# Optimization experiments

Hardware: AMD Instinct MI355X
Metric: run time of the kernel (lower is better)

## Reference

```python
import jax, jax.numpy as jnp
import numpy as np

HEADS = 12
HEAD_DIM = 64
WINDOW = 65  # must be odd
EMBED = 768
B, L = 1, 2048


def setup_inputs() -> dict:
    key = jax.random.key(0)
    k1, k2, k3 = jax.random.split(key, 3)
    x = jax.random.normal(k1, (B, L, EMBED), dtype=jnp.float32)
    w_qkv = jax.random.normal(k2, (EMBED, 3 * HEADS * HEAD_DIM), dtype=jnp.float32) * 0.02
    w_out = jax.random.normal(k3, (HEADS * HEAD_DIM, EMBED), dtype=jnp.float32) * 0.02
    b_out = jnp.zeros((EMBED,), dtype=jnp.float32)
    return {"x": x, "w_qkv": w_qkv, "w_out": w_out, "b_out": b_out}


def reference(x, w_qkv, w_out, b_out):
    b, l, _ = x.shape
    pad = WINDOW // 2
    # qkv projection (no bias), reshape to [B, L, H, 3*Dh], split as in TF code
    qkv = jnp.einsum('ble,ef->blf', x, w_qkv).reshape(b, l, HEADS, 3 * HEAD_DIM)
    q = qkv[..., :HEAD_DIM]                      # [B, L, H, Dh]
    k = qkv[..., HEAD_DIM:2 * HEAD_DIM]
    v = qkv[..., 2 * HEAD_DIM:]
    # zero-pad along sequence (matches tf.pad; padded positions participate in softmax)
    k_pad = jnp.pad(k, ((0, 0), (pad, pad), (0, 0), (0, 0)))  # [B, L+2p, H, Dh]
    v_pad = jnp.pad(v, ((0, 0), (pad, pad), (0, 0), (0, 0)))
    # sliding windows via a single gather: [B, L, W, H, Dh]
    idx = jnp.arange(l)[:, None] + jnp.arange(WINDOW)[None, :]
    k_win = k_pad[:, idx]
    v_win = v_pad[:, idx]
    score = jnp.einsum('blhd,blwhd->blhw', q, k_win) / jnp.sqrt(
        jnp.asarray(HEAD_DIM, dtype=x.dtype))
    weights = jax.nn.softmax(score, axis=-1)      # [B, L, H, W]
    out = jnp.einsum('blhw,blwhd->blhd', weights, v_win)
    out = out.reshape(b, l, HEADS * HEAD_DIM)
    return jnp.einsum('blf,fe->ble', out, w_out) + b_out
```

## Files before the change

### kernel.cpp

```cpp
#include <hip/hip_runtime.h>
#include <hip/hip_bf16.h>

#define HEADS 12
#define HD 64
#define PADW 32
#define EMBED 768
#define LSEQ 2048
#define QKV_N (3 * HEADS * HD)
#define LPAD (LSEQ + 64)

typedef short short8 __attribute__((ext_vector_type(8)));
typedef short short4v __attribute__((ext_vector_type(4)));
typedef float f32x4 __attribute__((ext_vector_type(4)));

__device__ short g_xb[LSEQ * EMBED];
__device__ short g_wqkvT[QKV_N * EMBED];
__device__ short g_woutT[EMBED * EMBED];
__device__ short g_qkvb[LSEQ * QKV_N];
__device__ short g_vT[HEADS * HD * LPAD];
__device__ short g_attnb[LSEQ * EMBED];

__device__ __forceinline__ short f2bf(float f) {
  unsigned x = __builtin_bit_cast(unsigned, f);
  x += 0x7fffu + ((x >> 16) & 1u);
  return (short)(x >> 16);
}

#define GLB(p) ((const __attribute__((address_space(1))) void*)(p))
#define LDS(p) ((__attribute__((address_space(3))) void*)(p))

#define PREP_A 1536
#define PREP_B 1728
#define PREP_C 576
#define PREP_D 24
#define PREP_TOT (PREP_A + PREP_B + PREP_C + PREP_D)

__global__ __launch_bounds__(256) void prep(
    const float* __restrict__ x, const float* __restrict__ w_qkv,
    const float* __restrict__ w_out, short* __restrict__ xb,
    short* __restrict__ wqkvT, short* __restrict__ woutT,
    short* __restrict__ vT) {
  __shared__ float T[32][33];
  const int b = blockIdx.x, tid = threadIdx.x;
  if (b < PREP_A) {
    int i = b * 256 + tid;
    float4 v = ((const float4*)x)[i];
    short4v o;
    o[0] = f2bf(v.x); o[1] = f2bf(v.y); o[2] = f2bf(v.z); o[3] = f2bf(v.w);
    ((short4v*)xb)[i] = o;
  } else if (b < PREP_A + PREP_B + PREP_C) {
    const float* W; short* WT; int N, bx, by;
    if (b < PREP_A + PREP_B) {
      int t = b - PREP_A; W = w_qkv; WT = wqkvT; N = QKV_N; bx = t % 72; by = t / 72;
    } else {
      int t = b - PREP_A - PREP_B; W = w_out; WT = woutT; N = EMBED; bx = t % 24; by = t / 24;
    }
    const int K = EMBED;
    int tx = tid & 31, ty = tid >> 5;
    int n0 = bx * 32, k0 = by * 32;
#pragma unroll
    for (int p = 0; p < 4; ++p)
      T[ty + p * 8][tx] = W[(size_t)(k0 + ty + p * 8) * N + n0 + tx];
    __syncthreads();
#pragma unroll
    for (int p = 0; p < 4; ++p)
      WT[(size_t)(n0 + ty + p * 8) * K + k0 + tx] = f2bf(T[tx][ty + p * 8]);
  } else {
    int j = (b - PREP_A - PREP_B - PREP_C) * 256 + tid;
    int hd = j >> 3, side = (j >> 2) & 1, off = (j & 3) * 8;
    short8 z = {};
    *(short8*)&vT[(size_t)hd * LPAD + side * 2080 + off] = z;
  }
}

template <int BM, int BN, bool OUT_BF16, bool FUSE_VT>
__global__ __launch_bounds__(256) void gemm_pipe(
    const short* __restrict__ A, const short* __restrict__ Bt,
    const float* __restrict__ bias, void* __restrict__ Cv,
    short* __restrict__ vT, int M, int N, int K) {
  constexpr int MT = BM / 32, NT = BN / 32;
  constexpr int ACH = BM / 64, BCH = BN / 64;
  constexpr int SI = ACH + BCH;
  constexpr int BUF = (BM + BN) * 32;
  constexpr int EPI = OUT_BF16 ? BM * (BN + 16) : BM * (BN + 8) * 2;
  constexpr int LDSZ = (3 * BUF > EPI) ? 3 * BUF : EPI;
  __shared__ __align__(16) short lds_s[LDSZ];

  const int tid = threadIdx.x;
  const int wv = tid >> 6, lane = tid & 63;
  const int wm = wv >> 1, wn = wv & 1;
  const int lanelo = lane & 15, quad = lane >> 4;
  const int m0 = blockIdx.y * BM, n0 = blockIdx.x * BN;
  const int srow = lane >> 2, schk = lane & 3;

  f32x4 acc[MT][NT] = {};

  auto stage = [&](int j, int buf) {
    short* Ab = lds_s + buf * BUF;
    short* Bb = Ab + BM * 32;
    const int k0 = j * 32;
#pragma unroll
    for (int c = 0; c < ACH; ++c) {
      int chunk = wv * ACH + c;
      const short* ga = A + (size_t)(m0 + chunk * 16 + srow) * K + k0 + schk * 8;
      __builtin_amdgcn_global_load_lds(GLB(ga), LDS(&Ab[chunk * 16 * 32]), 16, 0, 0);
    }
#pragma unroll
    for (int c = 0; c < BCH; ++c) {
      int chunk = wv * BCH + c;
      const short* gb = Bt + (size_t)(n0 + chunk * 16 + srow) * K + k0 + schk * 8;
      __builtin_amdgcn_global_load_lds(GLB(gb), LDS(&Bb[chunk * 16 * 32]), 16, 0, 0);
    }
  };

  auto compute = [&](int buf) {
    short* Ab = lds_s + buf * BUF;
    short* Bb = Ab + BM * 32;
    short8 af[MT], bfr[NT];
#pragma unroll
    for (int mt = 0; mt < MT; ++mt)
      af[mt] = *(const short8*)&Ab[(wm * (MT * 16) + mt * 16 + lanelo) * 32 + quad * 8];
#pragma unroll
    for (int nt = 0; nt < NT; ++nt)
      bfr[nt] = *(const short8*)&Bb[(wn * (NT * 16) + nt * 16 + lanelo) * 32 + quad * 8];
    asm volatile("s_waitcnt lgkmcnt(0)" ::: "memory");
#pragma unroll
    for (int mt = 0; mt < MT; ++mt)
#pragma unroll
      for (int nt = 0; nt < NT; ++nt)
        acc[mt][nt] = __builtin_amdgcn_mfma_f32_16x16x32_bf16(af[mt], bfr[nt], acc[mt][nt], 0, 0, 0);
  };

  const int steps = K / 32;
  stage(0, 0);
  stage(1, 1);
  int cur = 0;
  for (int j = 0; j < steps - 1; ++j) {
    if constexpr (SI == 2)      asm volatile("s_waitcnt vmcnt(2)" ::: "memory");
    else if constexpr (SI == 3) asm volatile("s_waitcnt vmcnt(3)" ::: "memory");
    else                        asm volatile("s_waitcnt vmcnt(4)" ::: "memory");
    asm volatile("s_barrier" ::: "memory");
    if (j + 2 < steps) {
      int b2 = cur + 2; if (b2 >= 3) b2 -= 3;
      stage(j + 2, b2);
    }
    compute(cur);
    ++cur; if (cur == 3) cur = 0;
  }
  asm volatile("s_waitcnt vmcnt(0)" ::: "memory");
  asm volatile("s_barrier" ::: "memory");
  compute(cur);

  if (FUSE_VT) {
#pragma unroll
    for (int nt = 0; nt < NT; ++nt) {
      int c0 = n0 + wn * (NT * 16) + nt * 16;
      if ((c0 % 192) >= 128) {
        int h = c0 / 192, d0 = (c0 % 192) - 128;
#pragma unroll
        for (int mt = 0; mt < MT; ++mt) {
          int d = d0 + lanelo;
          int row0 = m0 + wm * (MT * 16) + mt * 16 + quad * 4;
          short4v o;
#pragma unroll
          for (int r = 0; r < 4; ++r) o[r] = f2bf(acc[mt][nt][r]);
          *(short4v*)&vT[(size_t)(h * 64 + d) * LPAD + PADW + row0] = o;
        }
      }
    }
  }

  __syncthreads();
  if (OUT_BF16) {
    constexpr int ST = BN + 16;
#pragma unroll
    for (int mt = 0; mt < MT; ++mt)
#pragma unroll
      for (int nt = 0; nt < NT; ++nt) {
        int rloc = wm * (MT * 16) + mt * 16 + quad * 4;
        int cloc = wn * (NT * 16) + nt * 16 + lanelo;
#pragma unroll
        for (int r = 0; r < 4; ++r)
          lds_s[(rloc + r) * ST + cloc] = f2bf(acc[mt][nt][r]);
      }
    __syncthreads();
    constexpr int TPR = BN / 8, RPP = 256 / TPR;
    short* Cc = (short*)Cv;
#pragma unroll
    for (int rp = 0; rp < BM; rp += RPP) {
      int row = rp + tid / TPR, seg = tid % TPR;
      short8 vv = *(const short8*)&lds_s[row * ST + seg * 8];
      *(short8*)&Cc[(size_t)(m0 + row) * N + n0 + seg * 8] = vv;
    }
  } else {
    constexpr int ST = BN + 8;
    float* fl = (float*)lds_s;
#pragma unroll
    for (int mt = 0; mt < MT; ++mt)
#pragma unroll
      for (int nt = 0; nt < NT; ++nt) {
        int rloc = wm * (MT * 16) + mt * 16 + quad * 4;
        int cloc = wn * (NT * 16) + nt * 16 + lanelo;
#pragma unroll
        for (int r = 0; r < 4; ++r)
          fl[(rloc + r) * ST + cloc] = acc[mt][nt][r];
      }
    __syncthreads();
    constexpr int TPR = BN / 4, RPP = 256 / TPR;
    float* Cc = (float*)Cv;
#pragma unroll
    for (int rp = 0; rp < BM; rp += RPP) {
      int row = rp + tid / TPR, seg = tid % TPR;
      float4 vv = *(const float4*)&fl[row * ST + seg * 4];
      float4 bb = *(const float4*)&bias[n0 + seg * 4];
      vv.x += bb.x; vv.y += bb.y; vv.z += bb.z; vv.w += bb.w;
      *(float4*)&Cc[(size_t)(m0 + row) * N + n0 + seg * 4] = vv;
    }
  }
}

__global__ __launch_bounds__(256) void attn_mfma(
    const short* __restrict__ qkvb, const short* __restrict__ vT,
    short* __restrict__ attnb) {
  const int blk = blockIdx.x;
  const int h = blk % HEADS;
  const int l0 = (blk / HEADS) * 64;
  const int sb = l0 - PADW;

  const int tid = threadIdx.x;
  const int wv = tid >> 6, lane = tid & 63;
  const int lanelo = lane & 15, quad = lane >> 4;
  const int qoff = h * 192, koff = h * 192 + 64;

  __shared__ __align__(16) short P_lds[64 * 136];

  const short* qp = qkvb + (size_t)(l0 + wv * 16 + lanelo) * QKV_N + qoff;
  short8 aq0 = *(const short8*)(qp + quad * 8);
  short8 aq1 = *(const short8*)(qp + 32 + quad * 8);

  f32x4 sacc[8] = {};
#pragma unroll
  for (int nt = 0; nt < 8; ++nt) {
    int gl = sb + nt * 16 + lanelo;
    short8 bk0 = {}, bk1 = {};
    if ((unsigned)gl < (unsigned)LSEQ) {
      const short* kp = qkvb + (size_t)gl * QKV_N + koff;
      bk0 = *(const short8*)(kp + quad * 8);
      bk1 = *(const short8*)(kp + 32 + quad * 8);
    }
    sacc[nt] = __builtin_amdgcn_mfma_f32_16x16x32_bf16(aq0, bk0, sacc[nt], 0, 0, 0);
    sacc[nt] = __builtin_amdgcn_mfma_f32_16x16x32_bf16(aq1, bk1, sacc[nt], 0, 0, 0);
  }

  short8 bv[4][4];
#pragma unroll
  for (int ks = 0; ks < 4; ++ks) {
    int lp = l0 + ks * 32 + quad * 8;
#pragma unroll
    for (int nt = 0; nt < 4; ++nt) {
      int d = nt * 16 + lanelo;
      bv[ks][nt] = *(const short8*)&vT[((size_t)h * 64 + d) * LPAD + lp];
    }
  }

  float rsum[4] = {0.f, 0.f, 0.f, 0.f};
#pragma unroll
  for (int nt = 0; nt < 8; ++nt)
#pragma unroll
    for (int r = 0; r < 4; ++r) {
      int li = wv * 16 + quad * 4 + r;
      int widx = nt * 16 + lanelo - li;
      float s = (widx >= 0 && widx <= 64) ? sacc[nt][r] * 0.125f : -1e30f;
      float p = __expf(s);
      sacc[nt][r] = p;
      rsum[r] += p;
    }
#pragma unroll
  for (int r = 0; r < 4; ++r) {
#pragma unroll
    for (int off = 1; off < 16; off <<= 1)
      rsum[r] += __shfl_xor(rsum[r], off);
    rsum[r] = 1.f / rsum[r];
  }
#pragma unroll
  for (int nt = 0; nt < 8; ++nt)
#pragma unroll
    for (int r = 0; r < 4; ++r) {
      int row = wv * 16 + quad * 4 + r;
      P_lds[row * 136 + nt * 16 + lanelo] = f2bf(sacc[nt][r] * rsum[r]);
    }
  __syncthreads();

  f32x4 oacc[4] = {};
#pragma unroll
  for (int ks = 0; ks < 4; ++ks) {
    short8 ap = *(const short8*)&P_lds[(wv * 16 + lanelo) * 136 + ks * 32 + quad * 8];
#pragma unroll
    for (int nt = 0; nt < 4; ++nt)
      oacc[nt] = __builtin_amdgcn_mfma_f32_16x16x32_bf16(ap, bv[ks][nt], oacc[nt], 0, 0, 0);
  }

  __syncthreads();
#pragma unroll
  for (int nt = 0; nt < 4; ++nt)
#pragma unroll
    for (int r = 0; r < 4; ++r) {
      int row = wv * 16 + quad * 4 + r;
      P_lds[row * 80 + nt * 16 + lanelo] = f2bf(oacc[nt][r]);
    }
  __syncthreads();
#pragma unroll
  for (int rp = 0; rp < 64; rp += 32) {
    int row = rp + tid / 8, seg = tid % 8;
    short8 vv = *(const short8*)&P_lds[row * 80 + seg * 8];
    *(short8*)&attnb[(size_t)(l0 + row) * EMBED + h * 64 + seg * 8] = vv;
  }
}

extern "C" void kernel_launch(void* const* d_in, const int* in_sizes, int n_in,
                              void* d_out, int out_size, void* d_ws, size_t ws_size,
                              hipStream_t stream) {
  const float* x     = (const float*)d_in[0];
  const float* w_qkv = (const float*)d_in[1];
  const float* w_out = (const float*)d_in[2];
  const float* b_out = (const float*)d_in[3];
  float* out = (float*)d_out;

  short *xb, *wqkvT, *woutT, *qkvb, *vT, *attnb;
  (void)hipGetSymbolAddress((void**)&xb,    HIP_SYMBOL(g_xb));
  (void)hipGetSymbolAddress((void**)&wqkvT, HIP_SYMBOL(g_wqkvT));
  (void)hipGetSymbolAddress((void**)&woutT, HIP_SYMBOL(g_woutT));
  (void)hipGetSymbolAddress((void**)&qkvb,  HIP_SYMBOL(g_qkvb));
  (void)hipGetSymbolAddress((void**)&vT,    HIP_SYMBOL(g_vT));
  (void)hipGetSymbolAddress((void**)&attnb, HIP_SYMBOL(g_attnb));

  prep<<<PREP_TOT, 256, 0, stream>>>(x, w_qkv, w_out, xb, wqkvT, woutT, vT);

  gemm_pipe<64, 64, true, true><<<dim3(QKV_N / 64, LSEQ / 64), 256, 0, stream>>>(
      xb, wqkvT, nullptr, qkvb, vT, LSEQ, QKV_N, EMBED);

  attn_mfma<<<(LSEQ / 64) * HEADS, 256, 0, stream>>>(qkvb, vT, attnb);

  gemm_pipe<64, 64, false, false><<<dim3(EMBED / 64, LSEQ / 64), 256, 0, stream>>>(
      attnb, woutT, b_out, out, nullptr, LSEQ, EMBED, EMBED);
}
```

Baseline: 120.4 us.

## Double GEMM K-step to 64 with XOR-swizzled LDS layout

The GEMM kernel is specialized to 64x64 tiles. Each pipeline stage now loads a K-slice of 64 instead of 32, halving the number of barrier/wait iterations and issuing two MFMA k-substeps per stage. LDS rows are stored with an XOR swizzle on the 16-byte chunk index to avoid bank conflicts in fragment reads. This raises LDS usage per block (three 16 KB buffers), which may reduce occupancy.

```diff
diff --git a/kernel.cpp b/kernel.cpp
--- a/kernel.cpp
+++ b/kernel.cpp
@@ -73,16 +73,13 @@
   }
 }
 
-template <int BM, int BN, bool OUT_BF16, bool FUSE_VT>
-__global__ __launch_bounds__(256) void gemm_pipe(
+template <bool OUT_BF16, bool FUSE_VT>
+__global__ __launch_bounds__(256) void gemm_pipe64(
     const short* __restrict__ A, const short* __restrict__ Bt,
     const float* __restrict__ bias, void* __restrict__ Cv,
     short* __restrict__ vT, int M, int N, int K) {
-  constexpr int MT = BM / 32, NT = BN / 32;
-  constexpr int ACH = BM / 64, BCH = BN / 64;
-  constexpr int SI = ACH + BCH;
-  constexpr int BUF = (BM + BN) * 32;
-  constexpr int EPI = OUT_BF16 ? BM * (BN + 16) : BM * (BN + 8) * 2;
+  constexpr int BUF = 2 * 64 * 64;
+  constexpr int EPI = OUT_BF16 ? 64 * 80 : 64 * 72 * 2;
   constexpr int LDSZ = (3 * BUF > EPI) ? 3 * BUF : EPI;
   __shared__ __align__(16) short lds_s[LDSZ];
 
@@ -90,55 +87,67 @@
   const int wv = tid >> 6, lane = tid & 63;
   const int wm = wv >> 1, wn = wv & 1;
   const int lanelo = lane & 15, quad = lane >> 4;
-  const int m0 = blockIdx.y * BM, n0 = blockIdx.x * BN;
-  const int srow = lane >> 2, schk = lane & 3;
-
-  f32x4 acc[MT][NT] = {};
+  const int m0 = blockIdx.y * 64, n0 = blockIdx.x * 64;
+  const int srow8 = lane >> 3, schk = lane & 7;
+  const int sgc = schk ^ srow8;
+  const int xk = lanelo & 7;
+
+  f32x4 acc[2][2] = {};
 
   auto stage = [&](int j, int buf) {
     short* Ab = lds_s + buf * BUF;
-    short* Bb = Ab + BM * 32;
-    const int k0 = j * 32;
-#pragma unroll
-    for (int c = 0; c < ACH; ++c) {
-      int chunk = wv * ACH + c;
-      const short* ga = A + (size_t)(m0 + chunk * 16 + srow) * K + k0 + schk * 8;
-      __builtin_amdgcn_global_load_lds(GLB(ga), LDS(&Ab[chunk * 16 * 32]), 16, 0, 0);
-    }
-#pragma unroll
-    for (int c = 0; c < BCH; ++c) {
-      int chunk = wv * BCH + c;
-      const short* gb = Bt + (size_t)(n0 + chunk * 16 + srow) * K + k0 + schk * 8;
-      __builtin_amdgcn_global_load_lds(GLB(gb), LDS(&Bb[chunk * 16 * 32]), 16, 0, 0);
+    short* Bb = Ab + 64 * 64;
+    const int k0 = j * 64;
+#pragma unroll
+    for (int c = 0; c < 2; ++c) {
+      int row = wv * 16 + c * 8 + srow8;
+      const short* ga = A + (size_t)(m0 + row) * K + k0 + sgc * 8;
+      __builtin_amdgcn_global_load_lds(GLB(ga), LDS(&Ab[(wv * 16 + c * 8) * 64]), 16, 0, 0);
+    }
+#pragma unroll
+    for (int c = 0; c < 2; ++c) {
+      int row = wv * 16 + c * 8 + srow8;
+      const short* gb = Bt + (size_t)(n0 + row) * K + k0 + sgc * 8;
+      __builtin_amdgcn_global_load_lds(GLB(gb), LDS(&Bb[(wv * 16 + c * 8) * 64]), 16, 0, 0);
     }
   };
 
   auto compute = [&](int buf) {
     short* Ab = lds_s + buf * BUF;
-    short* Bb = Ab + BM * 32;
-    short8 af[MT], bfr[NT];
-#pragma unroll
-    for (int mt = 0; mt < MT; ++mt)
-      af[mt] = *(const short8*)&Ab[(wm * (MT * 16) + mt * 16 + lanelo) * 32 + quad * 8];
-#pragma unroll
-    for (int nt = 0; nt < NT; ++nt)
-      bfr[nt] = *(const short8*)&Bb[(wn * (NT * 16) + nt * 16 + lanelo) * 32 + quad * 8];
+    short* Bb = Ab + 64 * 64;
+    short8 af[2][2], bfr[2][2];
+#pragma unroll
+    for (int ks = 0; ks < 2; ++ks) {
+#pragma unroll
+      for (int mt = 0; mt < 2; ++mt) {
+        int row = wm * 32 + mt * 16 + lanelo;
+        int p = (ks * 4 + quad) ^ xk;
+        af[ks][mt] = *(const short8*)&Ab[row * 64 + p * 8];
+      }
+#pragma unroll
+      for (int nt = 0; nt < 2; ++nt) {
+        int row = wn * 32 + nt * 16 + lanelo;
+        int p = (ks * 4 + quad) ^ xk;
+        bfr[ks][nt] = *(const short8*)&Bb[row * 64 + p * 8];
+      }
+    }
     asm volatile("s_waitcnt lgkmcnt(0)" ::: "memory");
 #pragma unroll
-    for (int mt = 0; mt < MT; ++mt)
-#pragma unroll
-      for (int nt = 0; nt < NT; ++nt)
-        acc[mt][nt] = __builtin_amdgcn_mfma_f32_16x16x32_bf16(af[mt], bfr[nt], acc[mt][nt], 0, 0, 0);
+    for (int ks = 0; ks < 2; ++ks)
+#pragma unroll
+      for (int mt = 0; mt < 2; ++mt)
+#pragma unroll
+        for (int nt = 0; nt < 2; ++nt)
+          acc[mt][nt] = __builtin_amdgcn_mfma_f32_16x16x32_bf16(
+              af[ks][mt], bfr[ks][nt], acc[mt][nt], 0, 0, 0);
   };
 
-  const int steps = K / 32;
+  const int steps = K / 64;
   stage(0, 0);
   stage(1, 1);
   int cur = 0;
   for (int j = 0; j < steps - 1; ++j) {
-    if constexpr (SI == 2)      asm volatile("s_waitcnt vmcnt(2)" ::: "memory");
-    else if constexpr (SI == 3) asm volatile("s_waitcnt vmcnt(3)" ::: "memory");
-    else                        asm volatile("s_waitcnt vmcnt(4)" ::: "memory");
+    asm volatile("s_waitcnt vmcnt(4)" ::: "memory");
     asm volatile("s_barrier" ::: "memory");
     if (j + 2 < steps) {
       int b2 = cur + 2; if (b2 >= 3) b2 -= 3;
@@ -153,14 +162,14 @@
 
   if (FUSE_VT) {
 #pragma unroll
-    for (int nt = 0; nt < NT; ++nt) {
-      int c0 = n0 + wn * (NT * 16) + nt * 16;
+    for (int nt = 0; nt < 2; ++nt) {
+      int c0 = n0 + wn * 32 + nt * 16;
       if ((c0 % 192) >= 128) {
         int h = c0 / 192, d0 = (c0 % 192) - 128;
 #pragma unroll
-        for (int mt = 0; mt < MT; ++mt) {
+        for (int mt = 0; mt < 2; ++mt) {
           int d = d0 + lanelo;
-          int row0 = m0 + wm * (MT * 16) + mt * 16 + quad * 4;
+          int row0 = m0 + wm * 32 + mt * 16 + quad * 4;
           short4v o;
 #pragma unroll
           for (int r = 0; r < 4; ++r) o[r] = f2bf(acc[mt][nt][r]);
@@ -172,45 +181,43 @@
 
   __syncthreads();
   if (OUT_BF16) {
-    constexpr int ST = BN + 16;
-#pragma unroll
-    for (int mt = 0; mt < MT; ++mt)
-#pragma unroll
-      for (int nt = 0; nt < NT; ++nt) {
-        int rloc = wm * (MT * 16) + mt * 16 + quad * 4;
-        int cloc = wn * (NT * 16) + nt * 16 + lanelo;
+    constexpr int ST = 80;
+#pragma unroll
+    for (int mt = 0; mt < 2; ++mt)
+#pragma unroll
+      for (int nt = 0; nt < 2; ++nt) {
+        int rloc = wm * 32 + mt * 16 + quad * 4;
+        int cloc = wn * 32 + nt * 16 + lanelo;
 #pragma unroll
         for (int r = 0; r < 4; ++r)
           lds_s[(rloc + r) * ST + cloc] = f2bf(acc[mt][nt][r]);
       }
     __syncthreads();
-    constexpr int TPR = BN / 8, RPP = 256 / TPR;
     short* Cc = (short*)Cv;
 #pragma unroll
-    for (int rp = 0; rp < BM; rp += RPP) {
-      int row = rp + tid / TPR, seg = tid % TPR;
+    for (int rp = 0; rp < 64; rp += 32) {
+      int row = rp + tid / 8, seg = tid % 8;
       short8 vv = *(const short8*)&lds_s[row * ST + seg * 8];
       *(short8*)&Cc[(size_t)(m0 + row) * N + n0 + seg * 8] = vv;
     }
   } else {
-    constexpr int ST = BN + 8;
+    constexpr int ST = 72;
     float* fl = (float*)lds_s;
 #pragma unroll
-    for (int mt = 0; mt < MT; ++mt)
-#pragma unroll
-      for (int nt = 0; nt < NT; ++nt) {
-        int rloc = wm * (MT * 16) + mt * 16 + quad * 4;
-        int cloc = wn * (NT * 16) + nt * 16 + lanelo;
+    for (int mt = 0; mt < 2; ++mt)
+#pragma unroll
+      for (int nt = 0; nt < 2; ++nt) {
+        int rloc = wm * 32 + mt * 16 + quad * 4;
+        int cloc = wn * 32 + nt * 16 + lanelo;
 #pragma unroll
         for (int r = 0; r < 4; ++r)
           fl[(rloc + r) * ST + cloc] = acc[mt][nt][r];
       }
     __syncthreads();
-    constexpr int TPR = BN / 4, RPP = 256 / TPR;
     float* Cc = (float*)Cv;
 #pragma unroll
-    for (int rp = 0; rp < BM; rp += RPP) {
-      int row = rp + tid / TPR, seg = tid % TPR;
+    for (int rp = 0; rp < 64; rp += 16) {
+      int row = rp + tid / 16, seg = tid % 16;
       float4 vv = *(const float4*)&fl[row * ST + seg * 4];
       float4 bb = *(const float4*)&bias[n0 + seg * 4];
       vv.x += bb.x; vv.y += bb.y; vv.z += bb.z; vv.w += bb.w;
@@ -336,11 +343,11 @@
 
   prep<<<PREP_TOT, 256, 0, stream>>>(x, w_qkv, w_out, xb, wqkvT, woutT, vT);
 
-  gemm_pipe<64, 64, true, true><<<dim3(QKV_N / 64, LSEQ / 64), 256, 0, stream>>>(
+  gemm_pipe64<true, true><<<dim3(QKV_N / 64, LSEQ / 64), 256, 0, stream>>>(
       xb, wqkvT, nullptr, qkvb, vT, LSEQ, QKV_N, EMBED);
 
   attn_mfma<<<(LSEQ / 64) * HEADS, 256, 0, stream>>>(qkvb, vT, attnb);
 
-  gemm_pipe<64, 64, false, false><<<dim3(EMBED / 64, LSEQ / 64), 256, 0, stream>>>(
+  gemm_pipe64<false, false><<<dim3(EMBED / 64, LSEQ / 64), 256, 0, stream>>>(
       attnb, woutT, b_out, out, nullptr, LSEQ, EMBED, EMBED);
 }
```

Result: faster. 112.8 us (-6.3%).
